# Kernel optimization log

Measured on AMD Instinct MI355X. Metric: run time of the kernel, lower is better.

## Reference

```python
import jax, jax.numpy as jnp
import numpy as np

N = 100000
E = 800000
NFEAT = 128
NHID = 128
NCLASS = 40
THRESHOLD = 0.1
EPS = 1e-8


def setup_inputs() -> dict:
    key = jax.random.key(0)
    ks = jax.random.split(key, 12)
    x = jax.random.normal(ks[0], (N, NFEAT), dtype=jnp.float32)
    edge_index = jax.random.randint(ks[1], (2, E), 0, N, dtype=jnp.int64)
    edge_index2 = jax.random.randint(ks[2], (2, E), 0, N, dtype=jnp.int64)
    s1 = 1.0 / np.sqrt(NFEAT)
    s2 = 1.0 / np.sqrt(NHID)
    s3 = 1.0 / np.sqrt(NCLASS)
    W_gc1 = jax.random.uniform(ks[3], (NFEAT, NHID), jnp.float32, -s1, s1)
    b_gc1 = jax.random.uniform(ks[4], (NHID,), jnp.float32, -s1, s1)
    W_gc2 = jax.random.uniform(ks[5], (NHID, NCLASS), jnp.float32, -s2, s2)
    b_gc2 = jax.random.uniform(ks[6], (NCLASS,), jnp.float32, -s2, s2)
    W_att1 = jax.random.uniform(ks[7], (NCLASS, NCLASS), jnp.float32, -s3, s3)
    b_att1 = jax.random.uniform(ks[8], (NCLASS,), jnp.float32, -s3, s3)
    W_att2 = jax.random.uniform(ks[9], (NCLASS, 1), jnp.float32, -s3, s3)
    return {"x": x, "W_gc1": W_gc1, "b_gc1": b_gc1, "W_gc2": W_gc2,
            "b_gc2": b_gc2, "W_att1": W_att1, "b_att1": b_att1,
            "W_att2": W_att2, "edge_index": edge_index, "edge_index2": edge_index2}


def att_coef(feat, row, col, alive):
    # cosine similarity per edge; edges failing the threshold get weight 0
    # (exactly equivalent to removing them: contribute 0 to degree & messages).
    a = feat[row]          # [E, d]
    b = feat[col]          # [E, d]
    dot = jnp.sum(a * b, axis=-1)
    na = jnp.maximum(jnp.linalg.norm(a, axis=-1), EPS)
    nb = jnp.maximum(jnp.linalg.norm(b, axis=-1), EPS)
    sims = dot / (na * nb)
    mask = alive & (sims >= THRESHOLD)
    # original computes this under torch.no_grad()
    ew = jax.lax.stop_gradient(jnp.where(mask, sims, 0.0))
    return ew, mask


def gcn_conv(x, row, col, ew, W, b):
    # PyG GCNConv with add_self_loops=True, normalize=True on weighted adjacency
    h = x @ W                                     # [N, out]
    deg = jax.ops.segment_sum(ew, row, num_segments=N) + 1.0  # +1 self loop
    dinv = deg ** -0.5
    nw = dinv[row] * ew * dinv[col]               # [E]
    agg = jax.ops.segment_sum(h[col] * nw[:, None], row, num_segments=N)
    agg = agg + h * (dinv * dinv)[:, None]        # self-loop contribution
    return agg + b


def reference(x, W_gc1, b_gc1, W_gc2, b_gc2, W_att1, b_att1, W_att2,
              edge_index, edge_index2):
    r1, c1 = edge_index[0], edge_index[1]
    r2, c2 = edge_index2[0], edge_index2[1]
    ones = jnp.ones((E,), dtype=bool)

    ew2, m2 = att_coef(x, r2, c2, ones)
    ew1, m1 = att_coef(x, r1, c1, ones)

    x2 = jax.nn.relu(gcn_conv(x, r2, c2, ew2, W_gc1, b_gc1))
    x1 = jax.nn.relu(gcn_conv(x, r1, c1, ew1, W_gc1, b_gc1))
    # dropout is identity at eval time

    ew2b, _ = att_coef(x2, r2, c2, m2)
    ew1b, _ = att_coef(x1, r1, c1, m1)

    x2 = gcn_conv(x2, r2, c2, ew2b, W_gc2, b_gc2)
    x1 = gcn_conv(x1, r1, c1, ew1b, W_gc2, b_gc2)

    z = jnp.stack([x1, x2], axis=1)               # [N, 2, C]
    w = jnp.tanh(z @ W_att1 + b_att1) @ W_att2    # [N, 2, 1]
    beta = jax.nn.softmax(w, axis=1)
    fused = jnp.sum(beta * z, axis=1)             # [N, C]
    return jax.nn.log_softmax(fused, axis=1)
```

## Files before the change

kernel.cpp:

```cpp
#include <hip/hip_runtime.h>
#include <hip/hip_bf16.h>

#define NN 100000
#define EE 800000
#define THRV 0.1f
#define DELTA 0.008f
#define EPSV 1e-8f

#define ATOMIC_ADD_F32 unsafeAtomicAdd

__device__ inline int dot4(int a, int b, int c) {
#if __has_builtin(__builtin_amdgcn_sdot4)
    return __builtin_amdgcn_sdot4(a, b, c, false);
#else
    int s = c;
    #pragma unroll
    for (int k = 0; k < 4; k++) {
        int av = (a << (24 - 8 * k)) >> 24;
        int bv = (b << (24 - 8 * k)) >> 24;
        s += av * bv;
    }
    return s;
#endif
}


__global__ __launch_bounds__(256) void normalize_k(const float* __restrict__ x,
                                                   unsigned short* __restrict__ xq,
                                                   float* __restrict__ rs,
                                                   float* __restrict__ norms_x,
                                                   float* __restrict__ degL1) {
    int node = blockIdx.x * 4 + (threadIdx.x >> 6);
    int lane = threadIdx.x & 63;
    float2 v = reinterpret_cast<const float2*>(x)[(size_t)node * 64 + lane];
    float ss = v.x * v.x + v.y * v.y;
    float am = fmaxf(fabsf(v.x), fabsf(v.y));
    #pragma unroll
    for (int off = 32; off; off >>= 1) {
        ss += __shfl_xor(ss, off);
        am = fmaxf(am, __shfl_xor(am, off));
    }
    float norm = fmaxf(sqrtf(ss), EPSV);
    am = fmaxf(am, 1e-12f);
    float qs = 127.0f / am;
    int q0 = __float2int_rn(v.x * qs);
    int q1 = __float2int_rn(v.y * qs);
    unsigned short packed = (unsigned short)((q0 & 0xff) | ((q1 & 0xff) << 8));
    xq[(size_t)node * 64 + lane] = packed;
    if (lane == 0) {
        norms_x[node] = norm;
        rs[node] = am / (127.0f * norm);
        degL1[node] = 1.0f;
        degL1[node + NN] = 1.0f;
    }
}


__global__ __launch_bounds__(256) void edge_sim1_k(
        const unsigned short* __restrict__ xq, const float* __restrict__ rs,
        const float* __restrict__ x, const float* __restrict__ norms_x,
        const int* __restrict__ r1, const int* __restrict__ c1,
        const int* __restrict__ r2, const int* __restrict__ c2,
        float* __restrict__ ews, float* __restrict__ degL1,
        int* __restrict__ cnt) {
    int tid = threadIdx.x;
    int e = blockIdx.x * 32 + (tid >> 3);
    int q = tid & 7;
    int rnode, cnode, gr;
    if (e < EE) { rnode = r1[e]; cnode = c1[e]; gr = rnode; }
    else { int ee = e - EE; rnode = r2[ee]; cnode = c2[ee]; gr = NN + rnode; }
    int role = q >> 2;
    int j = q & 3;
    int node = role ? cnode : rnode;
    const uint4* base = reinterpret_cast<const uint4*>(xq) + (size_t)node * 8 + j * 2;
    uint4 v0 = base[0];
    uint4 v1 = base[1];
    uint4 p0, p1;
    p0.x = (unsigned)__shfl_xor((int)v0.x, 4);
    p0.y = (unsigned)__shfl_xor((int)v0.y, 4);
    p0.z = (unsigned)__shfl_xor((int)v0.z, 4);
    p0.w = (unsigned)__shfl_xor((int)v0.w, 4);
    p1.x = (unsigned)__shfl_xor((int)v1.x, 4);
    p1.y = (unsigned)__shfl_xor((int)v1.y, 4);
    p1.z = (unsigned)__shfl_xor((int)v1.z, 4);
    p1.w = (unsigned)__shfl_xor((int)v1.w, 4);
    int d = dot4((int)v0.x, (int)p0.x, 0);
    d = dot4((int)v0.y, (int)p0.y, d);
    d = dot4((int)v0.z, (int)p0.z, d);
    d = dot4((int)v0.w, (int)p0.w, d);
    d = dot4((int)v1.x, (int)p1.x, d);
    d = dot4((int)v1.y, (int)p1.y, d);
    d = dot4((int)v1.z, (int)p1.z, d);
    d = dot4((int)v1.w, (int)p1.w, d);
    d += __shfl_xor(d, 1);
    d += __shfl_xor(d, 2);
    float sim = (float)d * rs[rnode] * rs[cnode];
    if (fabsf(sim - THRV) <= DELTA) {
        const float4* xa = reinterpret_cast<const float4*>(x + (size_t)rnode * 128);
        const float4* xb = reinterpret_cast<const float4*>(x + (size_t)cnode * 128);
        float df = 0.f;
        #pragma unroll
        for (int t = 0; t < 4; t++) {
            float4 a = xa[q + 8 * t];
            float4 b = xb[q + 8 * t];
            df += a.x * b.x + a.y * b.y + a.z * b.z + a.w * b.w;
        }
        df += __shfl_xor(df, 1);
        df += __shfl_xor(df, 2);
        df += __shfl_xor(df, 4);
        sim = df / (norms_x[rnode] * norms_x[cnode]);
    }
    float w = (sim >= THRV) ? sim : 0.0f;
    if (q == 0) {
        ews[e] = w;
        if (w != 0.0f) {
            ATOMIC_ADD_F32(&degL1[gr], w);
            atomicAdd(&cnt[gr], 1);
        }
    }
}


__global__ __launch_bounds__(512) void scan1_k(const int* __restrict__ in,
                                               int* __restrict__ out,
                                               int* __restrict__ partials, int n) {
    __shared__ int a[1024], b[1024];
    int t = threadIdx.x;
    int base = blockIdx.x * 1024;
    a[t]       = (base + t       < n) ? in[base + t]       : 0;
    a[t + 512] = (base + t + 512 < n) ? in[base + t + 512] : 0;
    __syncthreads();
    int* src = a; int* dst = b;
    for (int off = 1; off < 1024; off <<= 1) {
        #pragma unroll
        for (int q = 0; q < 2; q++) {
            int i = t + q * 512;
            int v = src[i];
            if (i >= off) v += src[i - off];
            dst[i] = v;
        }
        __syncthreads();
        int* tmp = src; src = dst; dst = tmp;
    }
    for (int q = 0; q < 2; q++) {
        int i = t + q * 512;
        if (base + i < n) out[base + i] = i ? src[i - 1] : 0;
    }
    if (t == 0) partials[blockIdx.x] = src[1023];
}

__global__ __launch_bounds__(256) void scan2_k(int* __restrict__ partials, int m) {
    __shared__ int a[256], b[256];
    int t = threadIdx.x;
    a[t] = (t < m) ? partials[t] : 0;
    __syncthreads();
    int* src = a; int* dst = b;
    for (int off = 1; off < 256; off <<= 1) {
        int v = src[t];
        if (t >= off) v += src[t - off];
        dst[t] = v;
        __syncthreads();
        int* tmp = src; src = dst; dst = tmp;
    }
    if (t < m) partials[t] = t ? src[t - 1] : 0;
}

__global__ void scan3_k(int* __restrict__ start, int* __restrict__ next,
                        const int* __restrict__ partials,
                        const int* __restrict__ cnt, int n) {
    int i = blockIdx.x * 256 + threadIdx.x;
    if (i < n) {
        int v = start[i] + partials[i >> 10];
        start[i] = v;
        next[i] = v;
        if (i == n - 1) start[n] = v + cnt[i];
    }
}


__global__ void scatter_alive_k(const int* __restrict__ r1, const int* __restrict__ c1,
                                const int* __restrict__ r2, const int* __restrict__ c2,
                                const float* __restrict__ ews,
                                const float* __restrict__ degL1,
                                int* __restrict__ next, int2* __restrict__ acw) {
    int e = blockIdx.x * 256 + threadIdx.x;
    float w = ews[e];
    if (w == 0.0f) return;
    int gr, c, sb;
    if (e < EE) { gr = r1[e]; c = c1[e]; sb = 0; }
    else        { gr = NN + r2[e - EE]; c = c2[e - EE]; sb = NN; }
    int pos = atomicAdd(&next[gr], 1);
    int2 rec;
    rec.x = c;
    rec.y = __float_as_int(w * rsqrtf(degL1[sb + c]));
    acw[pos] = rec;
}


__global__ __launch_bounds__(256) void gemm_nh_k(const float* __restrict__ A,
                                                 const float* __restrict__ W,
                                                 float* __restrict__ C, int n) {
    __shared__ float Ws[64 * 128];
    __shared__ float Xs[32 * 64];
    int tid = threadIdx.x;
    int row0 = blockIdx.x * 32;
    int cg = tid & 31;
    int rl = tid >> 5;
    float4 acc[4];
    #pragma unroll
    for (int i = 0; i < 4; i++) acc[i] = make_float4(0.f, 0.f, 0.f, 0.f);

    for (int kt = 0; kt < 2; kt++) {
        const float4* Wg = reinterpret_cast<const float4*>(W + kt * 64 * 128);
        float4* Ws4 = reinterpret_cast<float4*>(Ws);
        #pragma unroll
        for (int i = 0; i < 8; i++) Ws4[tid + 256 * i] = Wg[tid + 256 * i];
        float4* Xs4 = reinterpret_cast<float4*>(Xs);
        #pragma unroll
        for (int i = 0; i < 2; i++) {
            int idx = tid + 256 * i;
            int rr = idx >> 4, kq = idx & 15;
            int grow = row0 + rr; if (grow >= n) grow = n - 1;
            Xs4[idx] = reinterpret_cast<const float4*>(A + (size_t)grow * 128 + kt * 64)[kq];
        }
        __syncthreads();
        for (int k = 0; k < 64; k++) {
            float4 wv = reinterpret_cast<const float4*>(Ws + k * 128)[cg];
            #pragma unroll
            for (int r4 = 0; r4 < 4; r4++) {
                float xv = Xs[(rl + 8 * r4) * 64 + k];
                acc[r4].x += xv * wv.x; acc[r4].y += xv * wv.y;
                acc[r4].z += xv * wv.z; acc[r4].w += xv * wv.w;
            }
        }
        __syncthreads();
    }
    #pragma unroll
    for (int r4 = 0; r4 < 4; r4++) {
        int grow = row0 + rl + 8 * r4;
        if (grow < n) reinterpret_cast<float4*>(C + (size_t)grow * 128)[cg] = acc[r4];
    }
}


__global__ __launch_bounds__(256) void gemm_nc_k(const float* __restrict__ A,
                                                 const float* __restrict__ W,
                                                 float* __restrict__ C, int n) {
    __shared__ float Ws[128 * 40];
    __shared__ float Xs[64 * 130];
    int tid = threadIdx.x;
    int row0 = blockIdx.x * 64;
    for (int i = tid; i < 128 * 40; i += 256) Ws[i] = W[i];
    #pragma unroll
    for (int i = 0; i < 8; i++) {
        int idx = tid + 256 * i;
        int rr = idx >> 5, kq = idx & 31;
        int grow = row0 + rr; if (grow >= n) grow = n - 1;
        float4 v = reinterpret_cast<const float4*>(A + (size_t)grow * 128)[kq];
        float* dst = &Xs[rr * 130 + kq * 4];
        dst[0] = v.x; dst[1] = v.y; dst[2] = v.z; dst[3] = v.w;
    }
    __syncthreads();
    int c5 = tid & 7;
    int r  = tid >> 3;
    float acc0[5] = {0, 0, 0, 0, 0}, acc1[5] = {0, 0, 0, 0, 0};
    for (int k = 0; k < 128; k++) {
        float x0 = Xs[r * 130 + k], x1 = Xs[(r + 32) * 130 + k];
        #pragma unroll
        for (int c = 0; c < 5; c++) {
            float wv = Ws[k * 40 + c5 * 5 + c];
            acc0[c] += x0 * wv; acc1[c] += x1 * wv;
        }
    }
    int g0 = row0 + r, g1 = row0 + r + 32;
    if (g0 < n) {
        for (int c = 0; c < 5; c++) C[(size_t)g0 * 40 + c5 * 5 + c] = acc0[c];
    }
    if (g1 < n) {
        for (int c = 0; c < 5; c++) C[(size_t)g1 * 40 + c5 * 5 + c] = acc1[c];
    }
}


template<int WQ>
__global__ __launch_bounds__(256) void agg128_fused_k(
        const float* __restrict__ h, const int* __restrict__ start,
        const int2* __restrict__ acw, const float* __restrict__ degL1,
        const float* __restrict__ bias, float* __restrict__ agg,
        float* __restrict__ norms_l2, float* __restrict__ degL2,
        unsigned short* __restrict__ xq2, float* __restrict__ rs2) {
    int gr = blockIdx.x * 4 + (threadIdx.x >> 6);
    int lane = threadIdx.x & 63;
    int rnode = (gr < NN) ? gr : gr - NN;
    int j0 = start[gr], j1 = start[gr + 1];
    float2 acc = make_float2(0.f, 0.f);
    for (int j = j0; j < j1; j++) {
        int2 rec = acw[j];
        float wv = __int_as_float(rec.y);
        float2 hv = reinterpret_cast<const float2*>(h)[(size_t)rec.x * 64 + lane];
        acc.x += hv.x * wv;
        acc.y += hv.y * wv;
    }
    float dr = rsqrtf(degL1[gr]);
    float2 hs = reinterpret_cast<const float2*>(h)[(size_t)rnode * 64 + lane];
    float2 bb = reinterpret_cast<const float2*>(bias)[lane];
    float vx = fmaxf(acc.x * dr + hs.x * dr * dr + bb.x, 0.0f);
    float vy = fmaxf(acc.y * dr + hs.y * dr * dr + bb.y, 0.0f);
    reinterpret_cast<float2*>(agg)[(size_t)gr * 64 + lane] = make_float2(vx, vy);
    float ss = vx * vx + vy * vy;
    float am = fmaxf(vx, vy);
    #pragma unroll
    for (int off = 32; off; off >>= 1) {
        ss += __shfl_xor(ss, off);
        am = fmaxf(am, __shfl_xor(am, off));
    }
    float norm = fmaxf(sqrtf(ss), EPSV);
    if (WQ) {
        am = fmaxf(am, 1e-12f);
        float qs = 127.0f / am;
        int q0 = __float2int_rn(vx * qs);
        int q1 = __float2int_rn(vy * qs);
        xq2[(size_t)gr * 64 + lane] =
            (unsigned short)((q0 & 0xff) | ((q1 & 0xff) << 8));
        if (lane == 0) rs2[gr] = am / (127.0f * norm);
    }
    if (lane == 0) {
        norms_l2[gr] = norm;
        degL2[gr] = 1.0f;
    }
}


__global__ __launch_bounds__(256) void edge_sim2_k(
        const float* __restrict__ agg, const float* __restrict__ norms_l2,
        const int* __restrict__ start, int2* __restrict__ acw,
        float* __restrict__ degL2) {
    int gr = blockIdx.x * 4 + (threadIdx.x >> 6);
    int lane = threadIdx.x & 63;
    int j0 = start[gr], j1 = start[gr + 1];
    if (j0 == j1) return;
    int set_base = (gr < NN) ? 0 : NN;
    float2 a = reinterpret_cast<const float2*>(agg)[(size_t)gr * 64 + lane];
    float nr = norms_l2[gr];
    float sum = 0.f;
    for (int j = j0; j < j1; j++) {
        int2 rec = acw[j];
        int cg = set_base + rec.x;
        float2 b = reinterpret_cast<const float2*>(agg)[(size_t)cg * 64 + lane];
        float d = a.x * b.x + a.y * b.y;
        #pragma unroll
        for (int off = 32; off; off >>= 1) d += __shfl_xor(d, off);
        float sim = d / (nr * norms_l2[cg]);
        float w2 = (sim >= THRV) ? sim : 0.0f;
        if (lane == 0) acw[j].y = __float_as_int(w2);
        sum += w2;
    }
    if (lane == 0) degL2[gr] = 1.0f + sum;
}


__global__ __launch_bounds__(256) void edge_sim2_q_k(
        const unsigned short* __restrict__ xq2, const float* __restrict__ rs2,
        const float* __restrict__ agg, const float* __restrict__ norms_l2,
        const int* __restrict__ start, int2* __restrict__ acw,
        float* __restrict__ degL2) {
    int gr = blockIdx.x * 4 + (threadIdx.x >> 6);
    int lane = threadIdx.x & 63;
    int j0 = start[gr], j1 = start[gr + 1];
    if (j0 == j1) return;
    int set_base = (gr < NN) ? 0 : NN;
    unsigned int au = xq2[(size_t)gr * 64 + lane];
    int a0 = ((int)(au << 24)) >> 24;
    int a1 = ((int)(au << 16)) >> 24;
    float ra = rs2[gr];
    float nr = norms_l2[gr];
    float sum = 0.f;
    for (int j = j0; j < j1; j++) {
        int2 rec = acw[j];
        int cg = set_base + rec.x;
        unsigned int bu = xq2[(size_t)cg * 64 + lane];
        int b0 = ((int)(bu << 24)) >> 24;
        int b1 = ((int)(bu << 16)) >> 24;
        int d = a0 * b0 + a1 * b1;
        #pragma unroll
        for (int off = 32; off; off >>= 1) d += __shfl_xor(d, off);
        float sim = (float)d * ra * rs2[cg];
        if (fabsf(sim - THRV) <= DELTA) {
            float2 a = reinterpret_cast<const float2*>(agg)[(size_t)gr * 64 + lane];
            float2 b = reinterpret_cast<const float2*>(agg)[(size_t)cg * 64 + lane];
            float df = a.x * b.x + a.y * b.y;
            #pragma unroll
            for (int off = 32; off; off >>= 1) df += __shfl_xor(df, off);
            sim = df / (nr * norms_l2[cg]);
        }
        float w2 = (sim >= THRV) ? sim : 0.0f;
        if (lane == 0) acw[j].y = __float_as_int(w2);
        sum += w2;
    }
    if (lane == 0) degL2[gr] = 1.0f + sum;
}


__global__ __launch_bounds__(256) void agg40_fused_k(
        const float* __restrict__ h2, const int* __restrict__ start,
        const int2* __restrict__ acw, const float* __restrict__ degL2,
        const float* __restrict__ bias, float* __restrict__ aggy) {
    int gr = blockIdx.x * 4 + (threadIdx.x >> 6);
    int lane = threadIdx.x & 63;
    int set_base = (gr < NN) ? 0 : NN;
    int j0 = start[gr], j1 = start[gr + 1];
    bool act = lane < 40;
    float acc = 0.f;
    for (int j = j0; j < j1; j++) {
        int2 rec = acw[j];
        float w2 = __int_as_float(rec.y);
        if (w2 == 0.0f) continue;
        int cg = set_base + rec.x;
        float nv = w2 * rsqrtf(degL2[cg]);
        if (act) acc += h2[(size_t)cg * 40 + lane] * nv;
    }
    if (act) {
        float dr = rsqrtf(degL2[gr]);
        float self = h2[(size_t)gr * 40 + lane];
        aggy[(size_t)gr * 40 + lane] = acc * dr + self * dr * dr + bias[lane];
    }
}


__global__ __launch_bounds__(256) void fusion_k(const float* __restrict__ y1,
                                                const float* __restrict__ y2,
                                                const float* __restrict__ W1,
                                                const float* __restrict__ b1,
                                                const float* __restrict__ W2,
                                                float* __restrict__ out, int n) {
    __shared__ float W1s[40 * 40];
    __shared__ float b1s[40];
    __shared__ float W2s[40];
    int tid = threadIdx.x;
    for (int i = tid; i < 1600; i += 256) W1s[i] = W1[i];
    if (tid < 40) { b1s[tid] = b1[tid]; W2s[tid] = W2[tid]; }
    __syncthreads();
    int i = blockIdx.x * 256 + tid;
    if (i >= n) return;
    float z1[40], z2[40];
    const float4* y14 = reinterpret_cast<const float4*>(y1 + (size_t)i * 40);
    const float4* y24 = reinterpret_cast<const float4*>(y2 + (size_t)i * 40);
    #pragma unroll
    for (int q = 0; q < 10; q++) {
        float4 a = y14[q], b = y24[q];
        z1[4 * q] = a.x; z1[4 * q + 1] = a.y; z1[4 * q + 2] = a.z; z1[4 * q + 3] = a.w;
        z2[4 * q] = b.x; z2[4 * q + 1] = b.y; z2[4 * q + 2] = b.z; z2[4 * q + 3] = b.w;
    }
    float w1 = 0.f, w2 = 0.f;
    for (int c = 0; c < 40; c++) {
        float s1 = b1s[c], s2 = b1s[c];
        for (int j = 0; j < 40; j++) {
            float ww = W1s[j * 40 + c];
            s1 += z1[j] * ww; s2 += z2[j] * ww;
        }
        float wa = W2s[c];
        w1 += tanhf(s1) * wa; w2 += tanhf(s2) * wa;
    }
    float m = fmaxf(w1, w2);
    float e1 = expf(w1 - m), e2 = expf(w2 - m);
    float inv = 1.0f / (e1 + e2);
    float be1 = e1 * inv, be2 = e2 * inv;
    float fu[40];
    float mx = -1e30f;
    #pragma unroll
    for (int c = 0; c < 40; c++) {
        fu[c] = be1 * z1[c] + be2 * z2[c];
        mx = fmaxf(mx, fu[c]);
    }
    float se = 0.f;
    #pragma unroll
    for (int c = 0; c < 40; c++) se += expf(fu[c] - mx);
    float ls = logf(se);
    float4* o4 = reinterpret_cast<float4*>(out + (size_t)i * 40);
    #pragma unroll
    for (int q = 0; q < 10; q++) {
        float4 v;
        v.x = fu[4 * q] - mx - ls; v.y = fu[4 * q + 1] - mx - ls;
        v.z = fu[4 * q + 2] - mx - ls; v.w = fu[4 * q + 3] - mx - ls;
        o4[q] = v;
    }
}


extern "C" void kernel_launch(void* const* d_in, const int* in_sizes, int n_in,
                              void* d_out, int out_size, void* d_ws, size_t ws_size,
                              hipStream_t stream) {
    (void)in_sizes; (void)n_in; (void)out_size;
    const float* x   = (const float*)d_in[0];
    const float* Wg1 = (const float*)d_in[1];
    const float* bg1 = (const float*)d_in[2];
    const float* Wg2 = (const float*)d_in[3];
    const float* bg2 = (const float*)d_in[4];
    const float* Wa1 = (const float*)d_in[5];
    const float* ba1 = (const float*)d_in[6];
    const float* Wa2 = (const float*)d_in[7];
    const int* ei1 = (const int*)d_in[8];
    const int* ei2 = (const int*)d_in[9];
    const int *r1 = ei1, *c1 = ei1 + EE;
    const int *r2 = ei2, *c2 = ei2 + EE;
    float* out = (float*)d_out;

    float* wp = (float*)d_ws;
    float* norms_x  = wp;  wp += NN;
    float* norms_l2 = wp;  wp += 2 * NN;
    float* rs       = wp;  wp += NN;
    float* degL1    = wp;  wp += 2 * NN;
    float* degL2    = wp;  wp += 2 * NN;
    int*   cnt      = (int*)wp;  wp += 2 * NN;
    int*   start    = (int*)wp;  wp += 2 * NN + 8;
    int*   next     = (int*)wp;  wp += 2 * NN;
    int*   partials = (int*)wp;  wp += 512;
    float* ews      = wp;  wp += 2 * EE;
    int2*  acw      = (int2*)wp; wp += (size_t)2 * 2 * EE;
    float* h        = wp;  wp += (size_t)NN * 128;
    float* agg      = wp;  wp += (size_t)2 * NN * 128;
    float* rs2            = wp;
    unsigned short* xq2   = (unsigned short*)(wp + 2 * NN);
    size_t bytes_q = ((size_t)(wp - (float*)d_ws) + 2 * NN + (size_t)2 * NN * 32)
                     * sizeof(float);
    bool useq = ws_size >= bytes_q;

    unsigned short* xq = (unsigned short*)agg;
    float* h2   = h;
    float* aggy = agg;

    const int twoN = 2 * NN;
    const int twoE = 2 * EE;
    const int scan_blocks = (twoN + 1023) / 1024;

    (void)hipMemsetAsync(cnt, 0, sizeof(int) * twoN, stream);
    normalize_k<<<NN / 4, 256, 0, stream>>>(x, xq, rs, norms_x, degL1);
    edge_sim1_k<<<twoE / 32, 256, 0, stream>>>(xq, rs, x, norms_x,
                                               r1, c1, r2, c2, ews, degL1, cnt);

    scan1_k<<<scan_blocks, 512, 0, stream>>>(cnt, start, partials, twoN);
    scan2_k<<<1, 256, 0, stream>>>(partials, scan_blocks);
    scan3_k<<<(twoN + 255) / 256, 256, 0, stream>>>(start, next, partials, cnt, twoN);
    scatter_alive_k<<<twoE / 256, 256, 0, stream>>>(r1, c1, r2, c2, ews, degL1,
                                                    next, acw);

    gemm_nh_k<<<NN / 32, 256, 0, stream>>>(x, Wg1, h, NN);
    if (useq) {
        agg128_fused_k<1><<<twoN / 4, 256, 0, stream>>>(h, start, acw, degL1, bg1,
                                                        agg, norms_l2, degL2, xq2, rs2);
    } else {
        agg128_fused_k<0><<<twoN / 4, 256, 0, stream>>>(h, start, acw, degL1, bg1,
                                                        agg, norms_l2, degL2,
                                                        nullptr, nullptr);
    }

    if (useq) {
        edge_sim2_q_k<<<twoN / 4, 256, 0, stream>>>(xq2, rs2, agg, norms_l2,
                                                    start, acw, degL2);
    } else {
        edge_sim2_k<<<twoN / 4, 256, 0, stream>>>(agg, norms_l2, start, acw, degL2);
    }
    gemm_nc_k<<<twoN / 64, 256, 0, stream>>>(agg, Wg2, h2, twoN);
    agg40_fused_k<<<twoN / 4, 256, 0, stream>>>(h2, start, acw, degL2, bg2, aggy);

    fusion_k<<<(NN + 255) / 256, 256, 0, stream>>>(aggy, aggy + (size_t)NN * 40,
                                                   Wa1, ba1, Wa2, out, NN);
}
```

Baseline: 468.5 us.

## Store layer-1 hidden features in bf16 and drop int8 edge similarity path

The first GEMM now writes its output in bf16, and the layer-1 aggregation gathers the bf16 rows and converts them to float, which halves gather traffic for that stage. The int8-quantized edge similarity kernel and its quantization step in the aggregation kernel are removed, so the full fp32 edge_sim2_k always runs. h2 gets its own buffer instead of aliasing h. The bf16 rounding of h lowers precision ahead of the thresholded cosine similarity, and losing the int8 prefilter may make the second similarity pass more expensive.

Measured after the change: 461.7 us. About the same (-1.5%).

```diff
diff --git a/kernel.cpp b/kernel.cpp
--- a/kernel.cpp
+++ b/kernel.cpp
@@ -22,6 +22,16 @@
     }
     return s;
 #endif
+}
+
+__device__ inline unsigned short f2bf(float f) {
+    unsigned int u = __float_as_uint(f);
+    u += 0x7fffu + ((u >> 16) & 1u);
+    return (unsigned short)(u >> 16);
+}
+
+__device__ inline float bf2f(unsigned short s) {
+    return __uint_as_float(((unsigned int)s) << 16);
 }
 
 
@@ -199,7 +209,7 @@
 
 __global__ __launch_bounds__(256) void gemm_nh_k(const float* __restrict__ A,
                                                  const float* __restrict__ W,
-                                                 float* __restrict__ C, int n) {
+                                                 unsigned short* __restrict__ Cb, int n) {
     __shared__ float Ws[64 * 128];
     __shared__ float Xs[32 * 64];
     int tid = threadIdx.x;
@@ -238,7 +248,12 @@
     #pragma unroll
     for (int r4 = 0; r4 < 4; r4++) {
         int grow = row0 + rl + 8 * r4;
-        if (grow < n) reinterpret_cast<float4*>(C + (size_t)grow * 128)[cg] = acc[r4];
+        if (grow < n) {
+            ushort4 o;
+            o.x = f2bf(acc[r4].x); o.y = f2bf(acc[r4].y);
+            o.z = f2bf(acc[r4].z); o.w = f2bf(acc[r4].w);
+            reinterpret_cast<ushort4*>(Cb + (size_t)grow * 128)[cg] = o;
+        }
     }
 }
 
@@ -282,13 +297,11 @@
 }
 
 
-template<int WQ>
 __global__ __launch_bounds__(256) void agg128_fused_k(
-        const float* __restrict__ h, const int* __restrict__ start,
+        const unsigned short* __restrict__ hb, const int* __restrict__ start,
         const int2* __restrict__ acw, const float* __restrict__ degL1,
         const float* __restrict__ bias, float* __restrict__ agg,
-        float* __restrict__ norms_l2, float* __restrict__ degL2,
-        unsigned short* __restrict__ xq2, float* __restrict__ rs2) {
+        float* __restrict__ norms_l2, float* __restrict__ degL2) {
     int gr = blockIdx.x * 4 + (threadIdx.x >> 6);
     int lane = threadIdx.x & 63;
     int rnode = (gr < NN) ? gr : gr - NN;
@@ -297,35 +310,25 @@
     for (int j = j0; j < j1; j++) {
         int2 rec = acw[j];
         float wv = __int_as_float(rec.y);
-        float2 hv = reinterpret_cast<const float2*>(h)[(size_t)rec.x * 64 + lane];
-        acc.x += hv.x * wv;
-        acc.y += hv.y * wv;
+        unsigned int hv = reinterpret_cast<const unsigned int*>(hb)
+                              [(size_t)rec.x * 64 + lane];
+        acc.x += bf2f((unsigned short)(hv & 0xffff)) * wv;
+        acc.y += bf2f((unsigned short)(hv >> 16)) * wv;
     }
     float dr = rsqrtf(degL1[gr]);
-    float2 hs = reinterpret_cast<const float2*>(h)[(size_t)rnode * 64 + lane];
+    unsigned int hs = reinterpret_cast<const unsigned int*>(hb)
+                          [(size_t)rnode * 64 + lane];
+    float hx = bf2f((unsigned short)(hs & 0xffff));
+    float hy = bf2f((unsigned short)(hs >> 16));
     float2 bb = reinterpret_cast<const float2*>(bias)[lane];
-    float vx = fmaxf(acc.x * dr + hs.x * dr * dr + bb.x, 0.0f);
-    float vy = fmaxf(acc.y * dr + hs.y * dr * dr + bb.y, 0.0f);
+    float vx = fmaxf(acc.x * dr + hx * dr * dr + bb.x, 0.0f);
+    float vy = fmaxf(acc.y * dr + hy * dr * dr + bb.y, 0.0f);
     reinterpret_cast<float2*>(agg)[(size_t)gr * 64 + lane] = make_float2(vx, vy);
     float ss = vx * vx + vy * vy;
-    float am = fmaxf(vx, vy);
-    #pragma unroll
-    for (int off = 32; off; off >>= 1) {
-        ss += __shfl_xor(ss, off);
-        am = fmaxf(am, __shfl_xor(am, off));
-    }
-    float norm = fmaxf(sqrtf(ss), EPSV);
-    if (WQ) {
-        am = fmaxf(am, 1e-12f);
-        float qs = 127.0f / am;
-        int q0 = __float2int_rn(vx * qs);
-        int q1 = __float2int_rn(vy * qs);
-        xq2[(size_t)gr * 64 + lane] =
-            (unsigned short)((q0 & 0xff) | ((q1 & 0xff) << 8));
-        if (lane == 0) rs2[gr] = am / (127.0f * norm);
-    }
+    #pragma unroll
+    for (int off = 32; off; off >>= 1) ss += __shfl_xor(ss, off);
     if (lane == 0) {
-        norms_l2[gr] = norm;
+        norms_l2[gr] = fmaxf(sqrtf(ss), EPSV);
         degL2[gr] = 1.0f;
     }
 }
@@ -359,48 +362,6 @@
 }
 
 
-__global__ __launch_bounds__(256) void edge_sim2_q_k(
-        const unsigned short* __restrict__ xq2, const float* __restrict__ rs2,
-        const float* __restrict__ agg, const float* __restrict__ norms_l2,
-        const int* __restrict__ start, int2* __restrict__ acw,
-        float* __restrict__ degL2) {
-    int gr = blockIdx.x * 4 + (threadIdx.x >> 6);
-    int lane = threadIdx.x & 63;
-    int j0 = start[gr], j1 = start[gr + 1];
-    if (j0 == j1) return;
-    int set_base = (gr < NN) ? 0 : NN;
-    unsigned int au = xq2[(size_t)gr * 64 + lane];
-    int a0 = ((int)(au << 24)) >> 24;
-    int a1 = ((int)(au << 16)) >> 24;
-    float ra = rs2[gr];
-    float nr = norms_l2[gr];
-    float sum = 0.f;
-    for (int j = j0; j < j1; j++) {
-        int2 rec = acw[j];
-        int cg = set_base + rec.x;
-        unsigned int bu = xq2[(size_t)cg * 64 + lane];
-        int b0 = ((int)(bu << 24)) >> 24;
-        int b1 = ((int)(bu << 16)) >> 24;
-        int d = a0 * b0 + a1 * b1;
-        #pragma unroll
-        for (int off = 32; off; off >>= 1) d += __shfl_xor(d, off);
-        float sim = (float)d * ra * rs2[cg];
-        if (fabsf(sim - THRV) <= DELTA) {
-            float2 a = reinterpret_cast<const float2*>(agg)[(size_t)gr * 64 + lane];
-            float2 b = reinterpret_cast<const float2*>(agg)[(size_t)cg * 64 + lane];
-            float df = a.x * b.x + a.y * b.y;
-            #pragma unroll
-            for (int off = 32; off; off >>= 1) df += __shfl_xor(df, off);
-            sim = df / (nr * norms_l2[cg]);
-        }
-        float w2 = (sim >= THRV) ? sim : 0.0f;
-        if (lane == 0) acw[j].y = __float_as_int(w2);
-        sum += w2;
-    }
-    if (lane == 0) degL2[gr] = 1.0f + sum;
-}
-
-
 __global__ __launch_bounds__(256) void agg40_fused_k(
         const float* __restrict__ h2, const int* __restrict__ start,
         const int2* __restrict__ acw, const float* __restrict__ degL2,
@@ -490,7 +451,7 @@
 extern "C" void kernel_launch(void* const* d_in, const int* in_sizes, int n_in,
                               void* d_out, int out_size, void* d_ws, size_t ws_size,
                               hipStream_t stream) {
-    (void)in_sizes; (void)n_in; (void)out_size;
+    (void)in_sizes; (void)n_in; (void)out_size; (void)ws_size;
     const float* x   = (const float*)d_in[0];
     const float* Wg1 = (const float*)d_in[1];
     const float* bg1 = (const float*)d_in[2];
@@ -517,16 +478,10 @@
     int*   partials = (int*)wp;  wp += 512;
     float* ews      = wp;  wp += 2 * EE;
     int2*  acw      = (int2*)wp; wp += (size_t)2 * 2 * EE;
-    float* h        = wp;  wp += (size_t)NN * 128;
+    unsigned short* hb = (unsigned short*)wp; wp += (size_t)NN * 64;
+    float* h2       = wp;  wp += (size_t)2 * NN * 40;
     float* agg      = wp;  wp += (size_t)2 * NN * 128;
-    float* rs2            = wp;
-    unsigned short* xq2   = (unsigned short*)(wp + 2 * NN);
-    size_t bytes_q = ((size_t)(wp - (float*)d_ws) + 2 * NN + (size_t)2 * NN * 32)
-                     * sizeof(float);
-    bool useq = ws_size >= bytes_q;
-
     unsigned short* xq = (unsigned short*)agg;
-    float* h2   = h;
     float* aggy = agg;
 
     const int twoN = 2 * NN;
@@ -544,22 +499,11 @@
     scatter_alive_k<<<twoE / 256, 256, 0, stream>>>(r1, c1, r2, c2, ews, degL1,
                                                     next, acw);
 
-    gemm_nh_k<<<NN / 32, 256, 0, stream>>>(x, Wg1, h, NN);
-    if (useq) {
-        agg128_fused_k<1><<<twoN / 4, 256, 0, stream>>>(h, start, acw, degL1, bg1,
-                                                        agg, norms_l2, degL2, xq2, rs2);
-    } else {
-        agg128_fused_k<0><<<twoN / 4, 256, 0, stream>>>(h, start, acw, degL1, bg1,
-                                                        agg, norms_l2, degL2,
-                                                        nullptr, nullptr);
-    }
-
-    if (useq) {
-        edge_sim2_q_k<<<twoN / 4, 256, 0, stream>>>(xq2, rs2, agg, norms_l2,
-                                                    start, acw, degL2);
-    } else {
-        edge_sim2_k<<<twoN / 4, 256, 0, stream>>>(agg, norms_l2, start, acw, degL2);
-    }
+    gemm_nh_k<<<NN / 32, 256, 0, stream>>>(x, Wg1, hb, NN);
+    agg128_fused_k<<<twoN / 4, 256, 0, stream>>>(hb, start, acw, degL1, bg1,
+                                                 agg, norms_l2, degL2);
+
+    edge_sim2_k<<<twoN / 4, 256, 0, stream>>>(agg, norms_l2, start, acw, degL2);
     gemm_nc_k<<<twoN / 64, 256, 0, stream>>>(agg, Wg2, h2, twoN);
     agg40_fused_k<<<twoN / 4, 256, 0, stream>>>(h2, start, acw, degL2, bg2, aggy);
 
```
